# Performance work log

Hardware: AMD Instinct MI355X
Metric: run time of the kernel (lower is better)

Reference implementation:

```python
import jax, jax.numpy as jnp
import numpy as np

B, C4, N, L4 = 8, 64, 512, 12
CQ = C4 // 4  # conv output channels


def setup_inputs() -> dict:
    key = jax.random.key(0)
    k_x, k_wc, k_bc, k_wg, k_bg = jax.random.split(key, 5)
    x = jax.random.normal(k_x, (B, C4, N, L4), dtype=jnp.float32)
    # Conv2d(in_dim, in_dim//4, kernel_size=(1,1)) -> pointwise: weight (CQ, C4)
    W_conv = jax.random.normal(k_wc, (CQ, C4), dtype=jnp.float32) / np.sqrt(C4)
    b_conv = jax.random.normal(k_bc, (CQ,), dtype=jnp.float32) * 0.01
    # Linear(in_dim, in_dim)
    W_gcn = jax.random.normal(k_wg, (C4, C4), dtype=jnp.float32) / np.sqrt(C4)
    b_gcn = jax.random.normal(k_bg, (C4,), dtype=jnp.float32) * 0.01
    return {"x": x, "W_conv": W_conv, "b_conv": b_conv, "W_gcn": W_gcn, "b_gcn": b_gcn}


def reference(x, W_conv, b_conv, W_gcn, b_gcn):
    # --- SpatioTemporalCorrelationComputation ---
    # 1x1 conv over channels: (b,c4,n,l) -> (b,cq,n,l)
    Fc = jnp.einsum('oc,bcnl->bonl', W_conv, x) + b_conv[None, :, None, None]
    Fl = Fc[:, :, :, -1]                                   # b,cq,n (last time step)
    xy = jnp.einsum('bcn,bcmt->bnmt', Fl, Fc)              # b,n,n,l4
    xx = jnp.sqrt(jnp.einsum('bcn,bcn->bc', Fl, Fl))       # b,cq
    yy = jnp.sqrt(jnp.einsum('bcnt,bcnt->bc', Fc, Fc))     # b,cq
    l2 = jnp.einsum('bc,bc->b', xx, yy)[:, None, None, None]
    S = xy / l2                                            # b,n,n,l4

    # --- RelationalFeatureExtraction ---
    # Loop-based R[:, :, :, k] = sum_j S[:,k,None,:,j] * F4[:,:,:,j]
    # is exactly this single contraction (Se expansion never materialized):
    R = jnp.einsum('bknj,bcnj->bcnk', S, x)                # b,c4,n,n

    # --- GraphOperation ---
    A = jax.nn.relu(jnp.tanh(jnp.max(R, axis=1)))          # b,n,n
    xg = jnp.einsum('bcnk,bkn->bck', R, A)                 # b,c4,n
    # Linear over channel dim: Fg[b,o,k] = sum_c xg[b,c,k] W[o,c] + bias[o]
    Fg = jnp.einsum('bck,oc->bok', xg, W_gcn) + b_gcn[None, :, None]
    return Fg[..., None]                                   # b,c4,n,1
```

## Files before the change

### kernel.cpp

```cpp
#include <hip/hip_runtime.h>
#include <hip/hip_bf16.h>
#include <math.h>

#define B    8
#define C4   64
#define CQ   16
#define NN   512
#define L4   12
#define NCH1 8
#define KT   128

#define O_TH   0
#define O_TL   (O_TH + (size_t)B*1024*NN/2)
#define O_T2H  (O_TL + (size_t)B*1024*NN/2)
#define O_T2L  (O_T2H + (size_t)B*NN*1024/2)
#define O_FL   (O_T2L + (size_t)B*NN*1024/2)
#define O_FLTH (O_FL + (size_t)B*CQ*NN)
#define O_FLTL (O_FLTH + (size_t)B*NN*16/2)
#define O_XX   (O_FLTL + (size_t)B*NN*16/2)
#define O_YY   (O_XX + B*CQ)
#define O_L2   (O_YY + B*CQ)
#define O_AH   (O_L2 + 16)
#define O_AL   (O_AH + (size_t)B*NN*NN/2)
#define O_XGP  (O_AL + (size_t)B*NN*NN/2)

typedef __attribute__((ext_vector_type(8))) short short8;
typedef __attribute__((ext_vector_type(4))) float floatx4;
typedef __attribute__((ext_vector_type(16))) float floatx16;

__device__ inline void split2(float x0, float x1, uint& hw, uint& lw) {
  uint u0 = __float_as_uint(x0), u1 = __float_as_uint(x1);
  uint h0 = u0 >> 16, h1 = u1 >> 16;
  float r0 = x0 - __uint_as_float(h0 << 16);
  float r1 = x1 - __uint_as_float(h1 << 16);
  hw = h0 | (h1 << 16);
  lw = (__float_as_uint(r0) >> 16) | ((__float_as_uint(r1) >> 16) << 16);
}

__global__ __launch_bounds__(256) void k1_fc(const float* __restrict__ x,
                                             const float* __restrict__ Wc,
                                             const float* __restrict__ bc,
                                             float* __restrict__ ws) {
  int blk = blockIdx.x;
  int b = blk >> 6;
  int n0 = (blk & 63) * NCH1;
  int t = threadIdx.x;
  __shared__ __align__(16) float xs[C4*NCH1*L4];
  __shared__ float wcs[CQ*65];
  __shared__ float bcs[CQ];
  __shared__ __align__(16) float fcs[NCH1*CQ*L4];

  for (int e = t; e < CQ*C4; e += 256) {
    int q = e >> 6, c = e & 63;
    wcs[q*65 + c] = Wc[e];
  }
  if (t < CQ) bcs[t] = bc[t];
  const float* xb = x + (size_t)b*C4*NN*L4 + (size_t)n0*L4;
  for (int f = t; f < (C4*NCH1*L4)/4; f += 256) {
    int c = f / (NCH1*L4/4);
    int r = f - c*(NCH1*L4/4);
    float4 v = *(const float4*)(xb + (size_t)c*NN*L4 + r*4);
    *(float4*)(xs + c*(NCH1*L4) + r*4) = v;
  }
  __syncthreads();
  {
    int q = t & 15, slot = t >> 4;
    float accv[6];
    #pragma unroll
    for (int i = 0; i < 6; ++i) accv[i] = bcs[q];
    for (int c = 0; c < C4; ++c) {
      float wv = wcs[q*65 + c];
      const float* xc = xs + c*(NCH1*L4);
      #pragma unroll
      for (int i = 0; i < 6; ++i) accv[i] += wv * xc[slot + 16*i];
    }
    #pragma unroll
    for (int i = 0; i < 6; ++i) {
      int nj = slot + 16*i;
      int nl = nj / L4, j = nj - nl*L4;
      fcs[nl*(CQ*L4) + q*L4 + j] = accv[i];
      if (j == L4-1) ws[O_FL + ((size_t)b*CQ + q)*NN + n0 + nl] = accv[i];
    }
  }
  __syncthreads();
  if (t < CQ) {
    float yy = 0.f, xx = 0.f;
    for (int nl = 0; nl < NCH1; ++nl) {
      #pragma unroll
      for (int j = 0; j < L4; ++j) { float v = fcs[nl*(CQ*L4) + t*L4 + j]; yy += v*v; }
      float w = fcs[nl*(CQ*L4) + t*L4 + (L4-1)];
      xx += w*w;
    }
    atomicAdd(ws + O_YY + b*CQ + t, yy);
    atomicAdd(ws + O_XX + b*CQ + t, xx);
  }
  {
    int c = t >> 2, q0 = (t & 3) * 4;
    float vals[4][NCH1];
    ushort* T2H = (ushort*)(ws + O_T2H);
    ushort* T2L = (ushort*)(ws + O_T2L);
    for (int nl = 0; nl < NCH1; ++nl) {
      float xr[L4];
      *(float4*)&xr[0] = *(const float4*)(xs + c*(NCH1*L4) + nl*L4);
      *(float4*)&xr[4] = *(const float4*)(xs + c*(NCH1*L4) + nl*L4 + 4);
      *(float4*)&xr[8] = *(const float4*)(xs + c*(NCH1*L4) + nl*L4 + 8);
      float tvp[4];
      #pragma unroll
      for (int i = 0; i < 4; ++i) {
        float a = 0.f;
        #pragma unroll
        for (int j = 0; j < L4; ++j) a += fcs[nl*(CQ*L4) + (q0+i)*L4 + j] * xr[j];
        tvp[i] = a;
        vals[i][nl] = a;
      }
      uint hw0, lw0, hw1, lw1;
      split2(tvp[0], tvp[1], hw0, lw0);
      split2(tvp[2], tvp[3], hw1, lw1);
      size_t off2 = ((size_t)b*NN + n0 + nl)*1024 + t*4;
      *(uint2*)(T2H + off2) = make_uint2(hw0, hw1);
      *(uint2*)(T2L + off2) = make_uint2(lw0, lw1);
    }
    ushort* TH = (ushort*)(ws + O_TH);
    ushort* TL = (ushort*)(ws + O_TL);
    #pragma unroll
    for (int i = 0; i < 4; ++i) {
      int m = c*16 + q0 + i;
      uint hw[4], lw[4];
      #pragma unroll
      for (int jj = 0; jj < 4; ++jj)
        split2(vals[i][2*jj], vals[i][2*jj+1], hw[jj], lw[jj]);
      size_t off = ((size_t)b*1024 + m)*NN + n0;
      *(uint4*)(TH + off) = make_uint4(hw[0], hw[1], hw[2], hw[3]);
      *(uint4*)(TL + off) = make_uint4(lw[0], lw[1], lw[2], lw[3]);
    }
  }
}

__global__ void k1b_l2(float* __restrict__ ws) {
  int t = threadIdx.x;
  __shared__ float s[B*CQ];
  s[t] = sqrtf(ws[O_XX + t]) * sqrtf(ws[O_YY + t]);
  __syncthreads();
  if (t < B) {
    float sum = 0.f;
    #pragma unroll
    for (int q = 0; q < CQ; ++q) sum += s[t*CQ + q];
    ws[O_L2 + t] = 1.0f / sum;
  }
}

__global__ __launch_bounds__(256) void k1c_flt(float* __restrict__ ws) {
  int idx = blockIdx.x*256 + threadIdx.x;
  int b = idx >> 9, k = idx & 511;
  const float* fl = ws + O_FL + (size_t)b*CQ*NN + k;
  ushort h[16], l[16];
  #pragma unroll
  for (int q = 0; q < CQ; ++q) {
    float v = fl[(size_t)q*NN];
    uint u = __float_as_uint(v);
    uint hh = u >> 16;
    float r = v - __uint_as_float(hh << 16);
    h[q] = (ushort)hh;
    l[q] = (ushort)(__float_as_uint(r) >> 16);
  }
  ushort* FH  = (ushort*)(ws + O_FLTH) + (size_t)idx*16;
  ushort* FLo = (ushort*)(ws + O_FLTL) + (size_t)idx*16;
  *(uint4*)(FH)      = *(uint4*)&h[0];
  *(uint4*)(FH + 8)  = *(uint4*)&h[8];
  *(uint4*)(FLo)     = *(uint4*)&l[0];
  *(uint4*)(FLo + 8) = *(uint4*)&l[8];
}

__global__ __launch_bounds__(256, 4) void k2_mfma(float* __restrict__ ws) {
  int id = blockIdx.x;
  int kh = id & 1;
  int nch = (id >> 1) & 63;
  int b = id >> 7;
  int t = threadIdx.x;
  int w = t >> 6, lane = t & 63;
  int col = lane & 31, half = lane >> 5;
  float l2inv = ws[O_L2 + b];
  const ushort* FltH = (const ushort*)(ws + O_FLTH);
  const ushort* FltL = (const ushort*)(ws + O_FLTL);
  short8 bhf[2], blf[2];
  int kcol[2];
  #pragma unroll
  for (int kt = 0; kt < 2; ++kt) {
    kcol[kt] = kh*256 + w*64 + kt*32 + col;
    size_t off = ((size_t)(b*NN + kcol[kt]))*16 + half*8;
    bhf[kt] = *(const short8*)(FltH + off);
    blf[kt] = *(const short8*)(FltL + off);
  }
  const ushort* T2H = (const ushort*)(ws + O_T2H) + ((size_t)b*NN + nch*8)*1024;
  const ushort* T2L = (const ushort*)(ws + O_T2L) + ((size_t)b*NN + nch*8)*1024;
  ushort* AH = (ushort*)(ws + O_AH) + ((size_t)b*NN + nch*8)*NN;
  ushort* AL = (ushort*)(ws + O_AL) + ((size_t)b*NN + nch*8)*NN;

  for (int i = 0; i < 8; ++i) {
    short8 ah[2], al[2];
    #pragma unroll
    for (int ct = 0; ct < 2; ++ct) {
      size_t off = (size_t)i*1024 + (ct*32 + col)*16 + half*8;
      ah[ct] = *(const short8*)(T2H + off);
      al[ct] = *(const short8*)(T2L + off);
    }
    floatx16 acc[2][2];
    #pragma unroll
    for (int ct = 0; ct < 2; ++ct)
      #pragma unroll
      for (int kt = 0; kt < 2; ++kt) {
        floatx16 a = {0.f,0.f,0.f,0.f,0.f,0.f,0.f,0.f,
                      0.f,0.f,0.f,0.f,0.f,0.f,0.f,0.f};
        a = __builtin_amdgcn_mfma_f32_32x32x16_bf16(ah[ct], bhf[kt], a, 0, 0, 0);
        a = __builtin_amdgcn_mfma_f32_32x32x16_bf16(ah[ct], blf[kt], a, 0, 0, 0);
        a = __builtin_amdgcn_mfma_f32_32x32x16_bf16(al[ct], bhf[kt], a, 0, 0, 0);
        acc[ct][kt] = a;
      }
    #pragma unroll
    for (int kt = 0; kt < 2; ++kt) {
      float m = acc[0][kt][0];
      #pragma unroll
      for (int ct = 0; ct < 2; ++ct)
        #pragma unroll
        for (int rg = 0; rg < 16; ++rg)
          if (ct + rg) m = fmaxf(m, acc[ct][kt][rg]);
      m = fmaxf(m, __shfl_xor(m, 32));
      float av = fmaxf(tanhf(m*l2inv), 0.f);
      uint u = __float_as_uint(av);
      uint hh = u >> 16;
      float r = av - __uint_as_float(hh << 16);
      ushort lv = (ushort)(__float_as_uint(r) >> 16);
      if (half == 0) {
        AH[(size_t)i*NN + kcol[kt]] = (ushort)hh;
        AL[(size_t)i*NN + kcol[kt]] = lv;
      }
    }
  }
}

__global__ __launch_bounds__(256, 4) void k3_mfma(float* __restrict__ ws) {
  int id = blockIdx.x;
  int kb = id & 7;
  int mbb = (id >> 3) & 7;
  int ns = (id >> 6) & 1;
  int b = id >> 7;
  int t = threadIdx.x;
  int lane = t & 63;
  int w = t >> 6;
  int mw = w >> 1, kw = w & 1;
  int row = lane & 15, quad = lane >> 4;

  __shared__ __align__(16) ushort Ah[128*32];
  __shared__ __align__(16) ushort Al[128*32];
  __shared__ __align__(16) ushort Bh[64*32];
  __shared__ __align__(16) ushort Bl[64*32];

  const ushort* TH = (const ushort*)(ws + O_TH) + ((size_t)b*1024 + mbb*128)*NN;
  const ushort* TL = (const ushort*)(ws + O_TL) + ((size_t)b*1024 + mbb*128)*NN;
  const ushort* AHp = (const ushort*)(ws + O_AH) + ((size_t)b*NN + kb*64)*NN;
  const ushort* ALp = (const ushort*)(ws + O_AL) + ((size_t)b*NN + kb*64)*NN;

  floatx4 acc[4][2];
  #pragma unroll
  for (int i = 0; i < 4; ++i)
    #pragma unroll
    for (int j = 0; j < 2; ++j) acc[i][j] = (floatx4){0.f, 0.f, 0.f, 0.f};

  for (int ksx = 0; ksx < 8; ++ksx) {
    int p0 = ns*256 + ksx*32;
    __syncthreads();
    #pragma unroll
    for (int i = 0; i < 2; ++i) {
      int f = t + 256*i;
      int m = f >> 2, seg = (f & 3) * 8;
      *(uint4*)(Ah + m*32 + seg) = *(const uint4*)(TH + (size_t)m*NN + p0 + seg);
      *(uint4*)(Al + m*32 + seg) = *(const uint4*)(TL + (size_t)m*NN + p0 + seg);
    }
    {
      int j = t >> 2, seg = (t & 3) * 8;
      *(uint4*)(Bh + j*32 + seg) = *(const uint4*)(AHp + (size_t)j*NN + p0 + seg);
      *(uint4*)(Bl + j*32 + seg) = *(const uint4*)(ALp + (size_t)j*NN + p0 + seg);
    }
    __syncthreads();
    short8 bh[2], bl[2];
    #pragma unroll
    for (int kt = 0; kt < 2; ++kt) {
      int jrow = kw*32 + kt*16 + row;
      bh[kt] = *(const short8*)(Bh + jrow*32 + quad*8);
      bl[kt] = *(const short8*)(Bl + jrow*32 + quad*8);
    }
    #pragma unroll
    for (int mt = 0; mt < 4; ++mt) {
      int mrow = mw*64 + mt*16 + row;
      short8 ah = *(const short8*)(Ah + mrow*32 + quad*8);
      short8 al = *(const short8*)(Al + mrow*32 + quad*8);
      #pragma unroll
      for (int kt = 0; kt < 2; ++kt) {
        acc[mt][kt] = __builtin_amdgcn_mfma_f32_16x16x32_bf16(ah, bh[kt], acc[mt][kt], 0, 0, 0);
        acc[mt][kt] = __builtin_amdgcn_mfma_f32_16x16x32_bf16(ah, bl[kt], acc[mt][kt], 0, 0, 0);
        acc[mt][kt] = __builtin_amdgcn_mfma_f32_16x16x32_bf16(al, bh[kt], acc[mt][kt], 0, 0, 0);
      }
    }
  }
  float l2inv = ws[O_L2 + b];
  const float* flb = ws + O_FL + (size_t)b*CQ*NN;
  float fl[2][4];
  #pragma unroll
  for (int kt = 0; kt < 2; ++kt) {
    int kcol = kb*64 + kw*32 + kt*16 + row;
    #pragma unroll
    for (int rg = 0; rg < 4; ++rg)
      fl[kt][rg] = flb[(size_t)(quad*4 + rg)*NN + kcol];
  }
  #pragma unroll
  for (int mt = 0; mt < 4; ++mt) {
    int c = mbb*8 + mw*4 + mt;
    #pragma unroll
    for (int kt = 0; kt < 2; ++kt) {
      float s = fl[kt][0]*acc[mt][kt][0] + fl[kt][1]*acc[mt][kt][1]
              + fl[kt][2]*acc[mt][kt][2] + fl[kt][3]*acc[mt][kt][3];
      s += __shfl_xor(s, 32);
      s += __shfl_xor(s, 16);
      if (quad == 0) {
        int kcol = kb*64 + kw*32 + kt*16 + row;
        ws[O_XGP + (((size_t)(b*2 + ns)*C4 + c)*NN) + kcol] = s * l2inv;
      }
    }
  }
}

__global__ __launch_bounds__(256) void k4_out(const float* __restrict__ Wg,
                                              const float* __restrict__ bg,
                                              const float* __restrict__ ws,
                                              float* __restrict__ out) {
  int blk = blockIdx.x;
  int b = blk >> 2, kc = blk & 3;
  int t = threadIdx.x;
  __shared__ float xg[C4][KT+1];
  __shared__ float wg[C4*C4];
  for (int e = t; e < C4*C4; e += 256) wg[e] = Wg[e];
  for (int e = t; e < C4*KT; e += 256) {
    int c = e >> 7, kk = e & (KT-1);
    xg[c][kk] = ws[O_XGP + (((size_t)(b*2 + 0)*C4 + c)*NN) + kc*KT + kk]
              + ws[O_XGP + (((size_t)(b*2 + 1)*C4 + c)*NN) + kc*KT + kk];
  }
  __syncthreads();
  int kk = t & (KT-1);
  int ohalf = t >> 7;
  for (int oi = 0; oi < 32; ++oi) {
    int o = ohalf*32 + oi;
    float acc = bg[o];
    #pragma unroll
    for (int c = 0; c < C4; ++c) acc += wg[o*C4 + c] * xg[c][kk];
    out[((size_t)(b*C4 + o))*NN + kc*KT + kk] = acc;
  }
}

extern "C" void kernel_launch(void* const* d_in, const int* in_sizes, int n_in,
                              void* d_out, int out_size, void* d_ws, size_t ws_size,
                              hipStream_t stream) {
  const float* x  = (const float*)d_in[0];
  const float* Wc = (const float*)d_in[1];
  const float* bc = (const float*)d_in[2];
  const float* Wg = (const float*)d_in[3];
  const float* bg = (const float*)d_in[4];
  float* ws  = (float*)d_ws;
  float* out = (float*)d_out;

  hipMemsetAsync(ws + O_XX, 0, (2*B*CQ + 16)*sizeof(float), stream);

  k1_fc   <<<B*64,   256, 0, stream>>>(x, Wc, bc, ws);
  k1b_l2  <<<1,      128, 0, stream>>>(ws);
  k1c_flt <<<16,     256, 0, stream>>>(ws);
  k2_mfma <<<B*128,  256, 0, stream>>>(ws);
  k3_mfma <<<B*128,  256, 0, stream>>>(ws);
  k4_out  <<<B*4,    256, 0, stream>>>(Wg, bg, ws, out);
}
```

Baseline: 165.3 us.

## Merge l2/flt kernels, drop k3 split-K, interleave batches across blocks

Merges the l2-normalisation kernel into the Fl transpose/split kernel, which removes one launch. k3 no longer splits the reduction dimension in two: each block loops over all 512 positions and writes xg directly, so k4 no longer sums two partials. Block indexing in k2 and k3 now puts the batch in the low bits, which changes how blocks map to CUs and caches. The cost is that k3 launches half as many blocks with twice the serial loop length, and its launch bound drops to 2 blocks per CU, so there is less parallelism and less latency hiding.

New measurement: 153.7 us. -7.0%, faster.

```diff
diff --git a/kernel.cpp b/kernel.cpp
--- a/kernel.cpp
+++ b/kernel.cpp
@@ -22,7 +22,7 @@
 #define O_L2   (O_YY + B*CQ)
 #define O_AH   (O_L2 + 16)
 #define O_AL   (O_AH + (size_t)B*NN*NN/2)
-#define O_XGP  (O_AL + (size_t)B*NN*NN/2)
+#define O_XG   (O_AL + (size_t)B*NN*NN/2)
 
 typedef __attribute__((ext_vector_type(8))) short short8;
 typedef __attribute__((ext_vector_type(4))) float floatx4;
@@ -136,21 +136,20 @@
   }
 }
 
-__global__ void k1b_l2(float* __restrict__ ws) {
-  int t = threadIdx.x;
-  __shared__ float s[B*CQ];
-  s[t] = sqrtf(ws[O_XX + t]) * sqrtf(ws[O_YY + t]);
-  __syncthreads();
-  if (t < B) {
-    float sum = 0.f;
-    #pragma unroll
-    for (int q = 0; q < CQ; ++q) sum += s[t*CQ + q];
-    ws[O_L2 + t] = 1.0f / sum;
-  }
-}
-
-__global__ __launch_bounds__(256) void k1c_flt(float* __restrict__ ws) {
-  int idx = blockIdx.x*256 + threadIdx.x;
+__global__ __launch_bounds__(256) void k1b_l2flt(float* __restrict__ ws) {
+  int t = threadIdx.x;
+  if (blockIdx.x == 0) {
+    __shared__ float s[B*CQ];
+    if (t < B*CQ) s[t] = sqrtf(ws[O_XX + t]) * sqrtf(ws[O_YY + t]);
+    __syncthreads();
+    if (t < B) {
+      float sum = 0.f;
+      #pragma unroll
+      for (int q = 0; q < CQ; ++q) sum += s[t*CQ + q];
+      ws[O_L2 + t] = 1.0f / sum;
+    }
+  }
+  int idx = blockIdx.x*256 + t;
   int b = idx >> 9, k = idx & 511;
   const float* fl = ws + O_FL + (size_t)b*CQ*NN + k;
   ushort h[16], l[16];
@@ -173,9 +172,10 @@
 
 __global__ __launch_bounds__(256, 4) void k2_mfma(float* __restrict__ ws) {
   int id = blockIdx.x;
-  int kh = id & 1;
-  int nch = (id >> 1) & 63;
-  int b = id >> 7;
+  int b = id & 7;
+  int rest = id >> 3;
+  int kh = rest & 1;
+  int nch = rest >> 1;
   int t = threadIdx.x;
   int w = t >> 6, lane = t & 63;
   int col = lane & 31, half = lane >> 5;
@@ -238,12 +238,12 @@
   }
 }
 
-__global__ __launch_bounds__(256, 4) void k3_mfma(float* __restrict__ ws) {
+__global__ __launch_bounds__(256, 2) void k3_mfma(float* __restrict__ ws) {
   int id = blockIdx.x;
-  int kb = id & 7;
-  int mbb = (id >> 3) & 7;
-  int ns = (id >> 6) & 1;
-  int b = id >> 7;
+  int b = id & 7;
+  int rest = id >> 3;
+  int kb = rest & 7;
+  int mbb = rest >> 3;
   int t = threadIdx.x;
   int lane = t & 63;
   int w = t >> 6;
@@ -266,8 +266,8 @@
     #pragma unroll
     for (int j = 0; j < 2; ++j) acc[i][j] = (floatx4){0.f, 0.f, 0.f, 0.f};
 
-  for (int ksx = 0; ksx < 8; ++ksx) {
-    int p0 = ns*256 + ksx*32;
+  for (int ksx = 0; ksx < 16; ++ksx) {
+    int p0 = ksx*32;
     __syncthreads();
     #pragma unroll
     for (int i = 0; i < 2; ++i) {
@@ -323,7 +323,7 @@
       s += __shfl_xor(s, 16);
       if (quad == 0) {
         int kcol = kb*64 + kw*32 + kt*16 + row;
-        ws[O_XGP + (((size_t)(b*2 + ns)*C4 + c)*NN) + kcol] = s * l2inv;
+        ws[O_XG + ((size_t)b*C4 + c)*NN + kcol] = s * l2inv;
       }
     }
   }
@@ -341,8 +341,7 @@
   for (int e = t; e < C4*C4; e += 256) wg[e] = Wg[e];
   for (int e = t; e < C4*KT; e += 256) {
     int c = e >> 7, kk = e & (KT-1);
-    xg[c][kk] = ws[O_XGP + (((size_t)(b*2 + 0)*C4 + c)*NN) + kc*KT + kk]
-              + ws[O_XGP + (((size_t)(b*2 + 1)*C4 + c)*NN) + kc*KT + kk];
+    xg[c][kk] = ws[O_XG + ((size_t)(b*C4 + c))*NN + kc*KT + kk];
   }
   __syncthreads();
   int kk = t & (KT-1);
@@ -369,10 +368,9 @@
 
   hipMemsetAsync(ws + O_XX, 0, (2*B*CQ + 16)*sizeof(float), stream);
 
-  k1_fc   <<<B*64,   256, 0, stream>>>(x, Wc, bc, ws);
-  k1b_l2  <<<1,      128, 0, stream>>>(ws);
-  k1c_flt <<<16,     256, 0, stream>>>(ws);
-  k2_mfma <<<B*128,  256, 0, stream>>>(ws);
-  k3_mfma <<<B*128,  256, 0, stream>>>(ws);
-  k4_out  <<<B*4,    256, 0, stream>>>(Wg, bg, ws, out);
-}
+  k1_fc    <<<B*64,   256, 0, stream>>>(x, Wc, bc, ws);
+  k1b_l2flt<<<16,     256, 0, stream>>>(ws);
+  k2_mfma  <<<B*128,  256, 0, stream>>>(ws);
+  k3_mfma  <<<B*64,   256, 0, stream>>>(ws);
+  k4_out   <<<B*4,    256, 0, stream>>>(Wg, bg, ws, out);
+}
```
